# Optimization experiments

Hardware: AMD Instinct MI355X
Metric: run time of the kernel (lower is better)

Reference implementation:

```python
import jax, jax.numpy as jnp
import numpy as np

D_MODEL = 768
D_FF = 3072
N_EXPERTS = 9  # num_experts + 1 (expert 0 is the common expert)


def setup_inputs() -> dict:
    key = jax.random.key(0)
    ks = jax.random.split(key, 7)
    scale = 0.02
    return {
        "x": jax.random.normal(ks[0], (2, 1024, D_MODEL), jnp.float32),
        "Ws": jax.random.normal(ks[1], (D_MODEL, N_EXPERTS), jnp.float32) * scale,
        "bs": jnp.zeros((N_EXPERTS,), jnp.float32),
        "W1": jax.random.normal(ks[2], (N_EXPERTS, D_MODEL, D_FF), jnp.float32) * scale,
        "b1": jnp.zeros((N_EXPERTS, D_FF), jnp.float32),
        "W2": jax.random.normal(ks[3], (N_EXPERTS, D_FF, D_MODEL), jnp.float32) * scale,
        "b2": jnp.zeros((N_EXPERTS, D_MODEL), jnp.float32),
    }


def reference(x, Ws, bs, W1, b1, W2, b2):
    B, S, d = x.shape
    xt = x.reshape(-1, d)  # [T, d]
    # top-1 switch router
    route_prob = jax.nn.softmax(xt @ Ws + bs, axis=-1)  # [T, E]
    p = jnp.max(route_prob, axis=-1)       # [T]
    routes = jnp.argmax(route_prob, axis=-1)  # [T]
    # dense grouped FFN: every expert on every token (reference baseline)
    h = jax.nn.gelu(jnp.einsum('td,edf->tef', xt, W1) + b1, approximate=False)  # [T, E, f]
    out = jnp.einsum('tef,efd->ted', h, W2) + b2  # [T, E, d]
    common = out[:, 0, :]  # common expert output for all tokens
    sel = jnp.take_along_axis(out, routes[:, None, None], axis=1)[:, 0, :]  # [T, d]
    # tokens routed to expert 0: common * (p / stop_grad(p))  (==common in fwd)
    scaling = (p / jax.lax.stop_gradient(p))[:, None]
    pe = p[:, None]
    final = jnp.where((routes == 0)[:, None],
                      common * scaling,
                      pe * sel + (1.0 - pe) * common)
    return final.reshape(B, S, d)
```

## Files before the change

kernel.cpp:

```cpp
#include <hip/hip_runtime.h>
#include <stdint.h>
#include <math.h>

#define T_TOK 2048
#define DM 768
#define DF 3072
#define NE 9

typedef unsigned short ushort_t;
typedef __attribute__((ext_vector_type(8))) __bf16 bf16x8;
typedef __attribute__((ext_vector_type(4))) float f32x4;

__device__ __forceinline__ unsigned short f2bf(float f) {
  union { float f; uint32_t u; } v; v.f = f;
  uint32_t u = v.u;
  u = u + 0x7fffu + ((u >> 16) & 1u);
  return (unsigned short)(u >> 16);
}

__device__ __forceinline__ void gl_lds16(const void* g, void* l) {
  __builtin_amdgcn_global_load_lds(
      (const __attribute__((address_space(1))) unsigned int*)g,
      (__attribute__((address_space(3))) unsigned int*)l, 16, 0, 0);
}

__global__ __launch_bounds__(256) void route_kernel(
    const float* __restrict__ x, const float* __restrict__ Ws,
    const float* __restrict__ bs, ushort_t* __restrict__ xb,
    float* __restrict__ p, int* __restrict__ routes,
    int* __restrict__ counts, int* __restrict__ lists) {
  const int wave = threadIdx.x >> 6, lane = threadIdx.x & 63;
  const int t = blockIdx.x * 4 + wave;
  const float* xr = x + (size_t)t * DM;
  const int d0 = lane * 12;
  float xv[12];
#pragma unroll
  for (int i = 0; i < 12; ++i) xv[i] = xr[d0 + i];
#pragma unroll
  for (int i = 0; i < 12; ++i) xb[(size_t)t * DM + d0 + i] = f2bf(xv[i]);
  float acc[NE];
#pragma unroll
  for (int e = 0; e < NE; ++e) acc[e] = 0.f;
#pragma unroll
  for (int i = 0; i < 12; ++i) {
    const float* wr = Ws + (size_t)(d0 + i) * NE;
#pragma unroll
    for (int e = 0; e < NE; ++e) acc[e] += xv[i] * wr[e];
  }
#pragma unroll
  for (int off = 32; off >= 1; off >>= 1)
#pragma unroll
    for (int e = 0; e < NE; ++e) acc[e] += __shfl_xor(acc[e], off);
  if (lane == 0) {
    float m = -1e30f; int am = 0;
#pragma unroll
    for (int e = 0; e < NE; ++e) {
      float l = acc[e] + bs[e];
      acc[e] = l;
      if (l > m) { m = l; am = e; }
    }
    float s = 0.f;
#pragma unroll
    for (int e = 0; e < NE; ++e) s += expf(acc[e] - m);
    p[t] = 1.0f / s;
    routes[t] = am;
    if (am != 0) {
      int pos = atomicAdd(&counts[am], 1);
      lists[(am - 1) * T_TOK + pos] = t;
    }
  }
}

__global__ __launch_bounds__(256) void transpose_conv(
    const float* __restrict__ in, ushort_t* __restrict__ out,
    int rows, int cols) {
  __shared__ float tile[32][33];
  const int e = blockIdx.z;
  const float* src = in + (size_t)e * rows * cols;
  ushort_t* dst = out + (size_t)e * rows * cols;
  const int c0 = blockIdx.x * 32, r0 = blockIdx.y * 32;
  const int tx = threadIdx.x & 31, ty = threadIdx.x >> 5;
#pragma unroll
  for (int i = 0; i < 32; i += 8)
    tile[ty + i][tx] = src[(size_t)(r0 + ty + i) * cols + (c0 + tx)];
  __syncthreads();
#pragma unroll
  for (int i = 0; i < 32; i += 8)
    dst[(size_t)(c0 + ty + i) * rows + (r0 + tx)] = f2bf(tile[tx][ty + i]);
}

template <int K, int N, bool PASS1>
__global__ __launch_bounds__(256) void ffn_gemm(
    const ushort_t* __restrict__ Asrc0, const ushort_t* __restrict__ AsrcS,
    const ushort_t* __restrict__ Btb, const float* __restrict__ bias,
    const int* __restrict__ counts, const int* __restrict__ lists,
    ushort_t* __restrict__ D0b, ushort_t* __restrict__ DSb,
    float* __restrict__ D0f, float* __restrict__ DSf) {
  const int e = blockIdx.z;
  const int cnt = (e == 0) ? T_TOK : counts[e];
  const int m0 = blockIdx.y * 128;
  if (m0 >= cnt) return;
  const int n0 = blockIdx.x * 128;
  const int* list = lists + (e - 1) * T_TOK;
  const ushort_t* Asrc = (e == 0) ? Asrc0 : AsrcS;

  __shared__ ushort_t As[128 * 64];
  __shared__ ushort_t Bs[128 * 64];

  const int tid = threadIdx.x;
  const int wave = tid >> 6, lane = tid & 63;
  const int g = lane >> 4, lr = lane & 15;

  const ushort_t* Bbase = Btb + ((size_t)e * N + n0) * K;

  const ushort_t* aSrcPtr[4];
  const ushort_t* bSrcPtr[4];
#pragma unroll
  for (int i = 0; i < 4; ++i) {
    int cidx = (wave * 4 + i) * 64 + lane;
    int row = cidx >> 3;
    int ch = (cidx & 7) ^ (row & 7);
    int mrow = m0 + row;
    int tok = (e == 0) ? mrow : list[mrow < cnt ? mrow : cnt - 1];
    aSrcPtr[i] = Asrc + (size_t)tok * K + ch * 8;
    bSrcPtr[i] = Bbase + (size_t)row * K + ch * 8;
  }

  f32x4 acc[4][4];
#pragma unroll
  for (int mi = 0; mi < 4; ++mi)
#pragma unroll
    for (int ni = 0; ni < 4; ++ni) acc[mi][ni] = (f32x4){0.f, 0.f, 0.f, 0.f};

  const int wm = wave >> 1, wn = wave & 1;
  const int swz = (lr & 7) << 4;

  for (int k0 = 0; k0 < K; k0 += 64) {
#pragma unroll
    for (int i = 0; i < 4; ++i)
      gl_lds16(aSrcPtr[i] + k0, &As[(wave * 4 + i) * 512]);
#pragma unroll
    for (int i = 0; i < 4; ++i)
      gl_lds16(bSrcPtr[i] + k0, &Bs[(wave * 4 + i) * 512]);
    __syncthreads();
#pragma unroll
    for (int kk = 0; kk < 2; ++kk) {
      bf16x8 af[4], bfv[4];
#pragma unroll
      for (int mi = 0; mi < 4; ++mi) {
        int row = wm * 64 + mi * 16 + lr;
        int off = row * 128 + ((kk * 64 + g * 16) ^ swz);
        af[mi] = *(const bf16x8*)((const char*)As + off);
      }
#pragma unroll
      for (int ni = 0; ni < 4; ++ni) {
        int row = wn * 64 + ni * 16 + lr;
        int off = row * 128 + ((kk * 64 + g * 16) ^ swz);
        bfv[ni] = *(const bf16x8*)((const char*)Bs + off);
      }
#pragma unroll
      for (int mi = 0; mi < 4; ++mi)
#pragma unroll
        for (int ni = 0; ni < 4; ++ni)
          acc[mi][ni] = __builtin_amdgcn_mfma_f32_16x16x32_bf16(
              af[mi], bfv[ni], acc[mi][ni], 0, 0, 0);
    }
    __syncthreads();
  }

#pragma unroll
  for (int mi = 0; mi < 4; ++mi) {
#pragma unroll
    for (int r = 0; r < 4; ++r) {
      const int mrow = m0 + wm * 64 + mi * 16 + g * 4 + r;
      if (mrow >= cnt) continue;
      const int tok = (e == 0) ? mrow : list[mrow];
#pragma unroll
      for (int ni = 0; ni < 4; ++ni) {
        const int col = n0 + wn * 64 + ni * 16 + lr;
        float v = acc[mi][ni][r] + bias[e * N + col];
        if constexpr (PASS1) {
          float gv = 0.5f * v * (1.0f + erff(v * 0.70710678118654752f));
          ushort_t* Dst = (e == 0) ? D0b : DSb;
          Dst[(size_t)tok * N + col] = f2bf(gv);
        } else {
          float* Dst = (e == 0) ? D0f : DSf;
          Dst[(size_t)tok * N + col] = v;
        }
      }
    }
  }
}

__global__ __launch_bounds__(256) void combine_kernel(
    const float* __restrict__ Ocm, const float* __restrict__ Osel,
    const float* __restrict__ p, const int* __restrict__ routes,
    float* __restrict__ out) {
  const int idx = blockIdx.x * blockDim.x + threadIdx.x;
  const int t = idx / (DM / 4);
  f32x4 cm = ((const f32x4*)Ocm)[idx];
  const int r = routes[t];
  f32x4 res;
  if (r == 0) {
    res = cm;
  } else {
    const float pe = p[t];
    f32x4 sl = ((const f32x4*)Osel)[idx];
    res = pe * sl + (1.0f - pe) * cm;
  }
  ((f32x4*)out)[idx] = res;
}

extern "C" void kernel_launch(void* const* d_in, const int* in_sizes, int n_in,
                              void* d_out, int out_size, void* d_ws,
                              size_t ws_size, hipStream_t stream) {
  const float* x  = (const float*)d_in[0];
  const float* Ws = (const float*)d_in[1];
  const float* bs = (const float*)d_in[2];
  const float* W1 = (const float*)d_in[3];
  const float* b1 = (const float*)d_in[4];
  const float* W2 = (const float*)d_in[5];
  const float* b2 = (const float*)d_in[6];
  float* out = (float*)d_out;
  char* ws = (char*)d_ws;

  constexpr size_t XB_OFF  = 0;
  constexpr size_t WTB_OFF = XB_OFF + (size_t)T_TOK * DM * 2;
  constexpr size_t H0_OFF  = WTB_OFF + (size_t)NE * DF * DM * 2;
  constexpr size_t HS_OFF  = H0_OFF + (size_t)T_TOK * DF * 2;
  constexpr size_t OC_OFF  = HS_OFF + (size_t)T_TOK * DF * 2;
  constexpr size_t OS_OFF  = OC_OFF + (size_t)T_TOK * DM * 4;
  constexpr size_t P_OFF   = OS_OFF + (size_t)T_TOK * DM * 4;
  constexpr size_t RT_OFF  = P_OFF + (size_t)T_TOK * 4;
  constexpr size_t CNT_OFF = RT_OFF + (size_t)T_TOK * 4;
  constexpr size_t LST_OFF = CNT_OFF + 64;

  ushort_t* xb   = (ushort_t*)(ws + XB_OFF);
  ushort_t* Wtb  = (ushort_t*)(ws + WTB_OFF);
  ushort_t* H0   = (ushort_t*)(ws + H0_OFF);
  ushort_t* Hsel = (ushort_t*)(ws + HS_OFF);
  float* Ocm     = (float*)(ws + OC_OFF);
  float* Osel    = (float*)(ws + OS_OFF);
  float* p       = (float*)(ws + P_OFF);
  int* routes    = (int*)(ws + RT_OFF);
  int* counts    = (int*)(ws + CNT_OFF);
  int* lists     = (int*)(ws + LST_OFF);

  hipMemsetAsync(counts, 0, 64, stream);
  route_kernel<<<T_TOK / 4, 256, 0, stream>>>(x, Ws, bs, xb, p, routes, counts,
                                              lists);
  transpose_conv<<<dim3(DF / 32, DM / 32, NE), 256, 0, stream>>>(W1, Wtb, DM,
                                                                 DF);
  ffn_gemm<DM, DF, true><<<dim3(DF / 128, T_TOK / 128, NE), 256, 0, stream>>>(
      xb, xb, Wtb, b1, counts, lists, H0, Hsel, nullptr, nullptr);
  transpose_conv<<<dim3(DM / 32, DF / 32, NE), 256, 0, stream>>>(W2, Wtb, DF,
                                                                 DM);
  ffn_gemm<DF, DM, false><<<dim3(DM / 128, T_TOK / 128, NE), 256, 0, stream>>>(
      H0, Hsel, Wtb, b2, counts, lists, nullptr, nullptr, Ocm, Osel);
  combine_kernel<<<(T_TOK * DM / 4) / 256, 256, 0, stream>>>(Ocm, Osel, p,
                                                             routes, out);
}
```

Baseline: 358.0 us.

## Vectorize conversions, widen transpose tiles, remap GEMM blocks across XCDs, shrink pass-2 tile

The router now writes bf16 x with 4-wide stores. The weight transpose moves to 64x64 tiles with float4 loads and ushort4 stores, cutting per-element memory traffic. The FFN GEMM gets a BM template parameter so pass 2 runs with 64-row tiles, giving more blocks to fill the GPU. It also swaps the grid's M/N axes and remaps block IDs round-robin across the 8 XCDs, so blocks sharing weights stay on the same L2. The tradeoff is less reuse within each pass-2 tile and some extra index arithmetic per block.

```diff
diff --git a/kernel.cpp b/kernel.cpp
--- a/kernel.cpp
+++ b/kernel.cpp
@@ -37,7 +37,12 @@
 #pragma unroll
   for (int i = 0; i < 12; ++i) xv[i] = xr[d0 + i];
 #pragma unroll
-  for (int i = 0; i < 12; ++i) xb[(size_t)t * DM + d0 + i] = f2bf(xv[i]);
+  for (int i = 0; i < 3; ++i) {
+    ushort4 s;
+    s.x = f2bf(xv[i * 4 + 0]); s.y = f2bf(xv[i * 4 + 1]);
+    s.z = f2bf(xv[i * 4 + 2]); s.w = f2bf(xv[i * 4 + 3]);
+    *(ushort4*)(xb + (size_t)t * DM + d0 + i * 4) = s;
+  }
   float acc[NE];
 #pragma unroll
   for (int e = 0; e < NE; ++e) acc[e] = 0.f;
@@ -73,62 +78,91 @@
 
 __global__ __launch_bounds__(256) void transpose_conv(
     const float* __restrict__ in, ushort_t* __restrict__ out,
-    int rows, int cols) {
-  __shared__ float tile[32][33];
+    int R, int C) {
+  __shared__ float tile[64][65];
   const int e = blockIdx.z;
-  const float* src = in + (size_t)e * rows * cols;
-  ushort_t* dst = out + (size_t)e * rows * cols;
-  const int c0 = blockIdx.x * 32, r0 = blockIdx.y * 32;
-  const int tx = threadIdx.x & 31, ty = threadIdx.x >> 5;
-#pragma unroll
-  for (int i = 0; i < 32; i += 8)
-    tile[ty + i][tx] = src[(size_t)(r0 + ty + i) * cols + (c0 + tx)];
+  const float* src = in + (size_t)e * R * C;
+  ushort_t* dst = out + (size_t)e * R * C;
+  const int c0 = blockIdx.x * 64, r0 = blockIdx.y * 64;
+  const int k = threadIdx.x & 15, g = threadIdx.x >> 4;
+#pragma unroll
+  for (int i = 0; i < 4; ++i) {
+    const float4 v =
+        *(const float4*)(src + (size_t)(r0 + g + i * 16) * C + c0 + k * 4);
+    tile[g + i * 16][k * 4 + 0] = v.x;
+    tile[g + i * 16][k * 4 + 1] = v.y;
+    tile[g + i * 16][k * 4 + 2] = v.z;
+    tile[g + i * 16][k * 4 + 3] = v.w;
+  }
   __syncthreads();
 #pragma unroll
-  for (int i = 0; i < 32; i += 8)
-    dst[(size_t)(c0 + ty + i) * rows + (r0 + tx)] = f2bf(tile[tx][ty + i]);
-}
-
-template <int K, int N, bool PASS1>
+  for (int i = 0; i < 4; ++i) {
+    const int c = g + i * 16;
+    ushort4 s;
+    s.x = f2bf(tile[k * 4 + 0][c]);
+    s.y = f2bf(tile[k * 4 + 1][c]);
+    s.z = f2bf(tile[k * 4 + 2][c]);
+    s.w = f2bf(tile[k * 4 + 3][c]);
+    *(ushort4*)(dst + (size_t)(c0 + c) * R + r0 + k * 4) = s;
+  }
+}
+
+template <int K, int N, int BM, bool PASS1>
 __global__ __launch_bounds__(256) void ffn_gemm(
     const ushort_t* __restrict__ Asrc0, const ushort_t* __restrict__ AsrcS,
     const ushort_t* __restrict__ Btb, const float* __restrict__ bias,
     const int* __restrict__ counts, const int* __restrict__ lists,
     ushort_t* __restrict__ D0b, ushort_t* __restrict__ DSb,
     float* __restrict__ D0f, float* __restrict__ DSf) {
-  const int e = blockIdx.z;
+  const unsigned hw =
+      (blockIdx.z * gridDim.y + blockIdx.y) * gridDim.x + blockIdx.x;
+  const unsigned nwg = gridDim.x * gridDim.y * gridDim.z;
+  const unsigned w = (hw & 7u) * (nwg >> 3) + (hw >> 3);
+  const int bx = w % gridDim.x;
+  const unsigned t1 = w / gridDim.x;
+  const int by = t1 % gridDim.y;
+  const int e = t1 / gridDim.y;
+
   const int cnt = (e == 0) ? T_TOK : counts[e];
-  const int m0 = blockIdx.y * 128;
+  const int m0 = bx * BM;
   if (m0 >= cnt) return;
-  const int n0 = blockIdx.x * 128;
+  const int n0 = by * 128;
   const int* list = lists + (e - 1) * T_TOK;
   const ushort_t* Asrc = (e == 0) ? Asrc0 : AsrcS;
 
-  __shared__ ushort_t As[128 * 64];
+  __shared__ ushort_t As[BM * 64];
   __shared__ ushort_t Bs[128 * 64];
 
   const int tid = threadIdx.x;
   const int wave = tid >> 6, lane = tid & 63;
   const int g = lane >> 4, lr = lane & 15;
+  constexpr int AI = BM / 32;
+  constexpr int MR = BM / 32;
 
   const ushort_t* Bbase = Btb + ((size_t)e * N + n0) * K;
 
-  const ushort_t* aSrcPtr[4];
+  const ushort_t* aSrcPtr[AI];
   const ushort_t* bSrcPtr[4];
 #pragma unroll
-  for (int i = 0; i < 4; ++i) {
-    int cidx = (wave * 4 + i) * 64 + lane;
+  for (int i = 0; i < AI; ++i) {
+    int cidx = (wave * AI + i) * 64 + lane;
     int row = cidx >> 3;
     int ch = (cidx & 7) ^ (row & 7);
     int mrow = m0 + row;
     int tok = (e == 0) ? mrow : list[mrow < cnt ? mrow : cnt - 1];
     aSrcPtr[i] = Asrc + (size_t)tok * K + ch * 8;
+  }
+#pragma unroll
+  for (int i = 0; i < 4; ++i) {
+    int cidx = (wave * 4 + i) * 64 + lane;
+    int row = cidx >> 3;
+    int ch = (cidx & 7) ^ (row & 7);
     bSrcPtr[i] = Bbase + (size_t)row * K + ch * 8;
   }
 
-  f32x4 acc[4][4];
-#pragma unroll
-  for (int mi = 0; mi < 4; ++mi)
+  f32x4 acc[MR][4];
+#pragma unroll
+  for (int mi = 0; mi < MR; ++mi)
 #pragma unroll
     for (int ni = 0; ni < 4; ++ni) acc[mi][ni] = (f32x4){0.f, 0.f, 0.f, 0.f};
 
@@ -137,18 +171,18 @@
 
   for (int k0 = 0; k0 < K; k0 += 64) {
 #pragma unroll
-    for (int i = 0; i < 4; ++i)
-      gl_lds16(aSrcPtr[i] + k0, &As[(wave * 4 + i) * 512]);
+    for (int i = 0; i < AI; ++i)
+      gl_lds16(aSrcPtr[i] + k0, &As[(wave * AI + i) * 512]);
 #pragma unroll
     for (int i = 0; i < 4; ++i)
       gl_lds16(bSrcPtr[i] + k0, &Bs[(wave * 4 + i) * 512]);
     __syncthreads();
 #pragma unroll
     for (int kk = 0; kk < 2; ++kk) {
-      bf16x8 af[4], bfv[4];
-#pragma unroll
-      for (int mi = 0; mi < 4; ++mi) {
-        int row = wm * 64 + mi * 16 + lr;
+      bf16x8 af[MR], bfv[4];
+#pragma unroll
+      for (int mi = 0; mi < MR; ++mi) {
+        int row = wm * (MR * 16) + mi * 16 + lr;
         int off = row * 128 + ((kk * 64 + g * 16) ^ swz);
         af[mi] = *(const bf16x8*)((const char*)As + off);
       }
@@ -159,7 +193,7 @@
         bfv[ni] = *(const bf16x8*)((const char*)Bs + off);
       }
 #pragma unroll
-      for (int mi = 0; mi < 4; ++mi)
+      for (int mi = 0; mi < MR; ++mi)
 #pragma unroll
         for (int ni = 0; ni < 4; ++ni)
           acc[mi][ni] = __builtin_amdgcn_mfma_f32_16x16x32_bf16(
@@ -169,10 +203,10 @@
   }
 
 #pragma unroll
-  for (int mi = 0; mi < 4; ++mi) {
+  for (int mi = 0; mi < MR; ++mi) {
 #pragma unroll
     for (int r = 0; r < 4; ++r) {
-      const int mrow = m0 + wm * 64 + mi * 16 + g * 4 + r;
+      const int mrow = m0 + wm * (MR * 16) + mi * 16 + g * 4 + r;
       if (mrow >= cnt) continue;
       const int tok = (e == 0) ? mrow : list[mrow];
 #pragma unroll
@@ -249,14 +283,16 @@
   hipMemsetAsync(counts, 0, 64, stream);
   route_kernel<<<T_TOK / 4, 256, 0, stream>>>(x, Ws, bs, xb, p, routes, counts,
                                               lists);
-  transpose_conv<<<dim3(DF / 32, DM / 32, NE), 256, 0, stream>>>(W1, Wtb, DM,
+  transpose_conv<<<dim3(DF / 64, DM / 64, NE), 256, 0, stream>>>(W1, Wtb, DM,
                                                                  DF);
-  ffn_gemm<DM, DF, true><<<dim3(DF / 128, T_TOK / 128, NE), 256, 0, stream>>>(
-      xb, xb, Wtb, b1, counts, lists, H0, Hsel, nullptr, nullptr);
-  transpose_conv<<<dim3(DM / 32, DF / 32, NE), 256, 0, stream>>>(W2, Wtb, DF,
+  ffn_gemm<DM, DF, 128, true>
+      <<<dim3(T_TOK / 128, DF / 128, NE), 256, 0, stream>>>(
+          xb, xb, Wtb, b1, counts, lists, H0, Hsel, nullptr, nullptr);
+  transpose_conv<<<dim3(DM / 64, DF / 64, NE), 256, 0, stream>>>(W2, Wtb, DF,
                                                                  DM);
-  ffn_gemm<DF, DM, false><<<dim3(DM / 128, T_TOK / 128, NE), 256, 0, stream>>>(
-      H0, Hsel, Wtb, b2, counts, lists, nullptr, nullptr, Ocm, Osel);
+  ffn_gemm<DF, DM, 64, false>
+      <<<dim3(T_TOK / 64, DM / 128, NE), 256, 0, stream>>>(
+          H0, Hsel, Wtb, b2, counts, lists, nullptr, nullptr, Ocm, Osel);
   combine_kernel<<<(T_TOK * DM / 4) / 256, 256, 0, stream>>>(Ocm, Osel, p,
                                                              routes, out);
 }
```

Measured after the change: 509.3 us. 42.3% more time.
